# Optimization experiments

Hardware: AMD Instinct MI355X
Metric: run time of the kernel (lower is better)

## Reference

```python
import jax, jax.numpy as jnp
import numpy as np
from jax import lax


def setup_inputs() -> dict:
    key = jax.random.key(0)
    k1, k2 = jax.random.split(key)
    B, T, H, L = 64, 512, 768, 400
    hidden_states = jax.random.normal(k1, (B, T, H), dtype=jnp.float32)
    text_labels_length = jax.random.randint(k2, (B,), 1, L, dtype=jnp.int32)
    return {
        "hidden_states": hidden_states,
        "text_labels_length": text_labels_length,
        "max_label_length": L,  # static python int (min(max(lengths), 400))
    }


def reference(hidden_states, text_labels_length, max_label_length):
    # hidden_states: [B, T, H]; last channel is the CIF firing weight alpha.
    B, T, H = hidden_states.shape
    L = int(max_label_length)
    dtype = hidden_states.dtype

    alpha = jax.nn.sigmoid(hidden_states[:, :, -1])                 # [B, T]
    lengths = jnp.minimum(text_labels_length, L).astype(dtype)      # clamp to max_label_length
    alpha_sum = alpha.sum(axis=1)                                   # [B]
    scale = lengths / alpha_sum
    alpha_p = alpha * scale[:, None]                                # [B, T]
    hs = hidden_states[:, :, :-1]                                   # [B, T, H-1]

    # scan over the first L timesteps (original loops k in range(max_label_length))
    a_seq = jnp.swapaxes(alpha_p[:, :L], 0, 1)                      # [L, B]
    h_seq = jnp.swapaxes(hs[:, :L], 0, 1)                           # [L, B, H-1]

    def step(carry, xs):
        a_r, s_r = carry                                            # [B], [B, H-1]
        ak, hk = xs                                                 # [B], [B, H-1]
        a_a = ak + a_r
        fired = a_a >= 1.0
        # accumulation weight this step: full alpha if not fired, else residual (1 - a_r)
        w = jnp.where(fired, 1.0 - a_r, ak)                         # [B]
        s_a_k = s_r + w[:, None] * hk                               # [B, H-1]
        a_r_new = jnp.where(fired, ak - (1.0 - a_r), a_a)           # [B]
        s_r_new = jnp.where(fired[:, None], a_r_new[:, None] * hk, s_a_k)
        return (a_r_new, s_r_new), s_a_k

    init = (jnp.zeros((B,), dtype), jnp.zeros((B, H - 1), dtype))
    _, s_a = lax.scan(step, init, (a_seq, h_seq))                   # [L, B, H-1]
    s_a = jnp.swapaxes(s_a, 0, 1)                                   # [B, L, H-1]

    n_hat = ((lengths - alpha_sum) ** 2).sum()
    return s_a, n_hat
```

## Files before the change

kernel.cpp:

```cpp
#include <hip/hip_runtime.h>
#include <math.h>

namespace {
constexpr int kB  = 64;
constexpr int kT  = 512;
constexpr int kH  = 768;
constexpr int kH4 = kH / 4;
constexpr int kHm = 767;
constexpr int kL  = 400;
constexpr int kC  = 8;
constexpr int kTC = kL / kC;
constexpr int kTh = 192;
}

__device__ __forceinline__ float sigmoidf_(float x) {
  return 1.0f / (1.0f + expf(-x));
}

__global__ __launch_bounds__(512) void k_rec(
    const float* __restrict__ hs, const int* __restrict__ labels,
    float* __restrict__ asum_ws, int* __restrict__ rstart_ws,
    int* __restrict__ cstart_ws, float4* __restrict__ wms) {
  __shared__ float a_lds[kT];
  __shared__ float red[kT];
  const int b = blockIdx.x;
  const int tid = threadIdx.x;

  float sig = sigmoidf_(hs[(size_t)b * kT * kH + (size_t)tid * kH + kHm]);
  a_lds[tid] = sig;
  red[tid] = sig;
  __syncthreads();
  for (int off = 256; off > 0; off >>= 1) {
    if (tid < off) red[tid] += red[tid + off];
    __syncthreads();
  }

  if (tid == 0) {
    const float as = red[0];
    asum_ws[b] = as;
    const int lab = labels[b];
    const float len = (float)(lab < kL ? lab : kL);
    const float scale = len / as;
    float a_r = 0.0f;
    int lfc = -1;
    float4* wb = wms + b * kL;
    for (int c = 0; c < kC; ++c) {
      cstart_ws[b * kC + c] = lfc < 0 ? 0 : lfc;
      int lf = -1;
      const int kbase = c * kTC;
#pragma unroll
      for (int kk = 0; kk < kTC; ++kk) {
        const int k = kbase + kk;
        const float ak = a_lds[k] * scale;
        const float a_a = ak + a_r;
        const bool fired = (a_a >= 1.0f);
        const float w   = fired ? (1.0f - a_r) : ak;
        const float arn = fired ? (ak - (1.0f - a_r)) : a_a;
        const float m   = fired ? arn : ak;
        const float sel = fired ? 0.0f : 1.0f;
        wb[k] = make_float4(w, m, sel, 0.0f);
        if (fired) lf = k;
        a_r = arn;
      }
      rstart_ws[b * kC + c] = lf >= 0 ? lf : kbase;
      if (lf >= 0) lfc = c;
    }
  }
}

__global__ __launch_bounds__(kTh) void k_q(
    const float* __restrict__ hs, const int* __restrict__ labels,
    const float* __restrict__ asum_ws, const int* __restrict__ rstart_ws,
    const float4* __restrict__ wms, float4* __restrict__ q_ws,
    float* __restrict__ out) {
  __shared__ float4 lw[kL];
  const int b = blockIdx.x, c = blockIdx.y, tid = threadIdx.x;

  for (int i = tid; i < kL; i += kTh) lw[i] = wms[b * kL + i];

  if (b == 0 && c == 0 && tid < kB) {
    const float as = asum_ws[tid];
    const int lab = labels[tid];
    const float len = (float)(lab < kL ? lab : kL);
    const float d = len - as;
    float v = d * d;
    for (int off = 32; off > 0; off >>= 1) v += __shfl_down(v, off, 64);
    if (tid == 0) out[(size_t)kB * kL * kHm] = v;
  }
  __syncthreads();

  const int r1 = __builtin_amdgcn_readfirstlane(rstart_ws[b * kC + c]);
  const int ce = c * kTC + kTC;
  const float4* __restrict__ px = (const float4*)(hs + (size_t)b * kT * kH) + tid;

  float4 s = make_float4(0.f, 0.f, 0.f, 0.f);
#pragma unroll 5
  for (int k = r1; k < ce; ++k) {
    const float4 x = px[(size_t)k * kH4];
    const float4 cf = lw[k];
    s.x = fmaf(cf.y, x.x, cf.z * s.x);
    s.y = fmaf(cf.y, x.y, cf.z * s.y);
    s.z = fmaf(cf.y, x.z, cf.z * s.z);
    s.w = fmaf(cf.y, x.w, cf.z * s.w);
  }
  q_ws[(size_t)(b * kC + c) * kH4 + tid] = s;
}

__global__ __launch_bounds__(kTh) void k_scan(
    const float* __restrict__ hs, const int* __restrict__ cstart_ws,
    const float4* __restrict__ wms, const float4* __restrict__ q_ws,
    float* __restrict__ out) {
  __shared__ float4 lw[kL];
  const int b = blockIdx.x, c = blockIdx.y, tid = threadIdx.x;

  for (int i = tid; i < kL; i += kTh) lw[i] = wms[b * kL + i];
  __syncthreads();

  const int cs = __builtin_amdgcn_readfirstlane(cstart_ws[b * kC + c]);

  float4 s = make_float4(0.f, 0.f, 0.f, 0.f);
  {
    const float4* qb = q_ws + (size_t)b * kC * kH4 + tid;
    float4 qv[kC - 1];
#pragma unroll
    for (int j = 0; j < kC - 1; ++j) qv[j] = qb[(size_t)j * kH4];
#pragma unroll
    for (int j = 0; j < kC - 1; ++j) {
      if (j >= cs && j < c) {
        s.x += qv[j].x; s.y += qv[j].y; s.z += qv[j].z; s.w += qv[j].w;
      }
    }
  }

  const int cb = c * kTC, ce = cb + kTC;
  const float4* __restrict__ px = (const float4*)(hs + (size_t)b * kT * kH) + tid;
  const int h0 = 4 * tid;
  float* __restrict__ po = out + (size_t)b * kL * kHm + h0;
  const bool w3 = (h0 + 3 < kHm);

#pragma unroll 10
  for (int k = cb; k < ce; ++k) {
    const float4 x = px[(size_t)k * kH4];
    const float4 cf = lw[k];
    const float o0 = fmaf(cf.x, x.x, s.x);
    const float o1 = fmaf(cf.x, x.y, s.y);
    const float o2 = fmaf(cf.x, x.z, s.z);
    const float o3 = fmaf(cf.x, x.w, s.w);
    float* r = po + (size_t)k * kHm;
    r[0] = o0; r[1] = o1; r[2] = o2;
    if (w3) r[3] = o3;
    s.x = fmaf(cf.y, x.x, cf.z * s.x);
    s.y = fmaf(cf.y, x.y, cf.z * s.y);
    s.z = fmaf(cf.y, x.z, cf.z * s.z);
    s.w = fmaf(cf.y, x.w, cf.z * s.w);
  }
}

extern "C" void kernel_launch(void* const* d_in, const int* in_sizes, int n_in,
                              void* d_out, int out_size, void* d_ws, size_t ws_size,
                              hipStream_t stream) {
  const float* hs     = (const float*)d_in[0];
  const int*   labels = (const int*)d_in[1];
  float* out = (float*)d_out;

  float*  asum_ws   = (float*)d_ws;
  int*    rstart_ws = (int*)((char*)d_ws + 256);
  int*    cstart_ws = (int*)((char*)d_ws + 2304);
  float4* wms       = (float4*)((char*)d_ws + 8192);
  float4* q_ws      = (float4*)((char*)d_ws + (512 << 10));

  k_rec<<<kB, 512, 0, stream>>>(hs, labels, asum_ws, rstart_ws, cstart_ws, wms);
  k_q<<<dim3(kB, kC), kTh, 0, stream>>>(hs, labels, asum_ws, rstart_ws, wms,
                                        q_ws, out);
  k_scan<<<dim3(kB, kC), kTh, 0, stream>>>(hs, cstart_ws, wms, q_ws, out);
}
```

Before: 56.84 us.

## Split output writes between q and scan kernels at last fire, double chunks

```diff
diff --git a/kernel.cpp b/kernel.cpp
--- a/kernel.cpp
+++ b/kernel.cpp
@@ -8,7 +8,7 @@
 constexpr int kH4 = kH / 4;
 constexpr int kHm = 767;
 constexpr int kL  = 400;
-constexpr int kC  = 8;
+constexpr int kC  = 16;
 constexpr int kTC = kL / kC;
 constexpr int kTh = 192;
 }
@@ -19,7 +19,7 @@
 
 __global__ __launch_bounds__(512) void k_rec(
     const float* __restrict__ hs, const int* __restrict__ labels,
-    float* __restrict__ asum_ws, int* __restrict__ rstart_ws,
+    float* __restrict__ asum_ws, int* __restrict__ lf_ws,
     int* __restrict__ cstart_ws, float4* __restrict__ wms) {
   __shared__ float a_lds[kT];
   __shared__ float red[kT];
@@ -62,7 +62,7 @@
         if (fired) lf = k;
         a_r = arn;
       }
-      rstart_ws[b * kC + c] = lf >= 0 ? lf : kbase;
+      lf_ws[b * kC + c] = lf;
       if (lf >= 0) lfc = c;
     }
   }
@@ -70,7 +70,7 @@
 
 __global__ __launch_bounds__(kTh) void k_q(
     const float* __restrict__ hs, const int* __restrict__ labels,
-    const float* __restrict__ asum_ws, const int* __restrict__ rstart_ws,
+    const float* __restrict__ asum_ws, const int* __restrict__ lf_ws,
     const float4* __restrict__ wms, float4* __restrict__ q_ws,
     float* __restrict__ out) {
   __shared__ float4 lw[kL];
@@ -89,15 +89,27 @@
   }
   __syncthreads();
 
-  const int r1 = __builtin_amdgcn_readfirstlane(rstart_ws[b * kC + c]);
-  const int ce = c * kTC + kTC;
+  const int lf = __builtin_amdgcn_readfirstlane(lf_ws[b * kC + c]);
+  const int cb = c * kTC, ce = cb + kTC;
+  const bool haslf = (lf >= 0);
+  const int start = haslf ? lf : cb;
+
   const float4* __restrict__ px = (const float4*)(hs + (size_t)b * kT * kH) + tid;
+  const int h0 = 4 * tid;
+  float* __restrict__ po = out + (size_t)b * kL * kHm + h0;
+  const bool w3 = (h0 + 3 < kHm);
 
   float4 s = make_float4(0.f, 0.f, 0.f, 0.f);
-#pragma unroll 5
-  for (int k = r1; k < ce; ++k) {
+  for (int k = start; k < ce; ++k) {
     const float4 x = px[(size_t)k * kH4];
     const float4 cf = lw[k];
+    if (haslf && k > lf) {
+      float* r = po + (size_t)k * kHm;
+      __builtin_nontemporal_store(fmaf(cf.x, x.x, s.x), r + 0);
+      __builtin_nontemporal_store(fmaf(cf.x, x.y, s.y), r + 1);
+      __builtin_nontemporal_store(fmaf(cf.x, x.z, s.z), r + 2);
+      if (w3) __builtin_nontemporal_store(fmaf(cf.x, x.w, s.w), r + 3);
+    }
     s.x = fmaf(cf.y, x.x, cf.z * s.x);
     s.y = fmaf(cf.y, x.y, cf.z * s.y);
     s.z = fmaf(cf.y, x.z, cf.z * s.z);
@@ -107,48 +119,46 @@
 }
 
 __global__ __launch_bounds__(kTh) void k_scan(
-    const float* __restrict__ hs, const int* __restrict__ cstart_ws,
-    const float4* __restrict__ wms, const float4* __restrict__ q_ws,
-    float* __restrict__ out) {
+    const float* __restrict__ hs, const int* __restrict__ lf_ws,
+    const int* __restrict__ cstart_ws, const float4* __restrict__ wms,
+    const float4* __restrict__ q_ws, float* __restrict__ out) {
   __shared__ float4 lw[kL];
   const int b = blockIdx.x, c = blockIdx.y, tid = threadIdx.x;
 
   for (int i = tid; i < kL; i += kTh) lw[i] = wms[b * kL + i];
   __syncthreads();
 
+  const int lf = __builtin_amdgcn_readfirstlane(lf_ws[b * kC + c]);
   const int cs = __builtin_amdgcn_readfirstlane(cstart_ws[b * kC + c]);
+  const int cb = c * kTC;
+  const int kend = (lf >= 0) ? lf : (cb + kTC - 1);
 
   float4 s = make_float4(0.f, 0.f, 0.f, 0.f);
   {
     const float4* qb = q_ws + (size_t)b * kC * kH4 + tid;
-    float4 qv[kC - 1];
-#pragma unroll
-    for (int j = 0; j < kC - 1; ++j) qv[j] = qb[(size_t)j * kH4];
-#pragma unroll
-    for (int j = 0; j < kC - 1; ++j) {
-      if (j >= cs && j < c) {
-        s.x += qv[j].x; s.y += qv[j].y; s.z += qv[j].z; s.w += qv[j].w;
-      }
+    for (int j = cs; j < c; ++j) {
+      const float4 q = qb[(size_t)j * kH4];
+      s.x += q.x; s.y += q.y; s.z += q.z; s.w += q.w;
     }
   }
 
-  const int cb = c * kTC, ce = cb + kTC;
   const float4* __restrict__ px = (const float4*)(hs + (size_t)b * kT * kH) + tid;
   const int h0 = 4 * tid;
   float* __restrict__ po = out + (size_t)b * kL * kHm + h0;
   const bool w3 = (h0 + 3 < kHm);
 
-#pragma unroll 10
-  for (int k = cb; k < ce; ++k) {
+#pragma unroll
+  for (int kk = 0; kk < kTC; ++kk) {
+    const int k = cb + kk;
     const float4 x = px[(size_t)k * kH4];
     const float4 cf = lw[k];
-    const float o0 = fmaf(cf.x, x.x, s.x);
-    const float o1 = fmaf(cf.x, x.y, s.y);
-    const float o2 = fmaf(cf.x, x.z, s.z);
-    const float o3 = fmaf(cf.x, x.w, s.w);
-    float* r = po + (size_t)k * kHm;
-    r[0] = o0; r[1] = o1; r[2] = o2;
-    if (w3) r[3] = o3;
+    if (k <= kend) {
+      float* r = po + (size_t)k * kHm;
+      __builtin_nontemporal_store(fmaf(cf.x, x.x, s.x), r + 0);
+      __builtin_nontemporal_store(fmaf(cf.x, x.y, s.y), r + 1);
+      __builtin_nontemporal_store(fmaf(cf.x, x.z, s.z), r + 2);
+      if (w3) __builtin_nontemporal_store(fmaf(cf.x, x.w, s.w), r + 3);
+    }
     s.x = fmaf(cf.y, x.x, cf.z * s.x);
     s.y = fmaf(cf.y, x.y, cf.z * s.y);
     s.z = fmaf(cf.y, x.z, cf.z * s.z);
@@ -164,13 +174,14 @@
   float* out = (float*)d_out;
 
   float*  asum_ws   = (float*)d_ws;
-  int*    rstart_ws = (int*)((char*)d_ws + 256);
-  int*    cstart_ws = (int*)((char*)d_ws + 2304);
-  float4* wms       = (float4*)((char*)d_ws + 8192);
-  float4* q_ws      = (float4*)((char*)d_ws + (512 << 10));
+  int*    lf_ws     = (int*)((char*)d_ws + 256);
+  int*    cstart_ws = (int*)((char*)d_ws + 4608);
+  float4* wms       = (float4*)((char*)d_ws + 16384);
+  float4* q_ws      = (float4*)((char*)d_ws + 442368);
 
-  k_rec<<<kB, 512, 0, stream>>>(hs, labels, asum_ws, rstart_ws, cstart_ws, wms);
-  k_q<<<dim3(kB, kC), kTh, 0, stream>>>(hs, labels, asum_ws, rstart_ws, wms,
-                                        q_ws, out);
-  k_scan<<<dim3(kB, kC), kTh, 0, stream>>>(hs, cstart_ws, wms, q_ws, out);
+  k_rec<<<kB, 512, 0, stream>>>(hs, labels, asum_ws, lf_ws, cstart_ws, wms);
+  k_q<<<dim3(kB, kC), kTh, 0, stream>>>(hs, labels, asum_ws, lf_ws, wms, q_ws,
+                                        out);
+  k_scan<<<dim3(kB, kC), kTh, 0, stream>>>(hs, lf_ws, cstart_ws, wms, q_ws,
+                                           out);
 }
```

Result: slower. 68.56 us (+20.6%).
